# Kernel optimization log

Measured on AMD Instinct MI355X. Metric: run time of the kernel, lower is better.

Reference implementation:

```python
import jax, jax.numpy as jnp
import numpy as np

B, N, E, D, L = 32, 400, 200, 768, 3  # batch, max_entities, max_evidences, emb_dim, num_layers
_REL = ["ev_att", "ent_att", "ev_ent", "ent_ent", "ent_ev", "ev_ev"]


def setup_inputs() -> dict:
    key = jax.random.key(0)
    ks = jax.random.split(key, 20)
    s = 0.02
    inp = {
        "ent_emb": jax.random.normal(ks[0], (B, N, D), jnp.float32),
        "ev_emb": jax.random.normal(ks[1], (B, E, D), jnp.float32),
        "sr_vec": jax.random.normal(ks[2], (B, D), jnp.float32),
        "adj": (jax.random.uniform(ks[3], (B, E, N)) < 0.05).astype(jnp.float32),
    }
    for i, r in enumerate(_REL):
        inp[f"W_{r}"] = jax.random.normal(ks[4 + i], (L, D, D), jnp.float32) * s
        inp[f"b_{r}"] = jnp.zeros((L, D), jnp.float32)
    inp["W_ans"] = jax.random.normal(ks[10], (D, D), jnp.float32) * s
    inp["b_ans"] = jnp.zeros((), jnp.float32)
    inp["W_evb"] = jax.random.normal(ks[11], (D, D), jnp.float32) * s
    inp["b_evb"] = jnp.zeros((), jnp.float32)
    return inp


def _lin(x, W, b):
    return jnp.einsum('b...d,de->b...e', x, W) + b


def reference(ent_emb, ev_emb, sr_vec, adj,
              W_ev_att, b_ev_att, W_ent_att, b_ent_att,
              W_ev_ent, b_ev_ent, W_ent_ent, b_ent_ent,
              W_ent_ev, b_ent_ev, W_ev_ev, b_ev_ev,
              W_ans, b_ans, W_evb, b_evb):
    eps = 1e-9
    # degree-normalized adjacency: ev->ent aggregation and ent->ev aggregation
    adj_en = adj / (adj.sum(axis=1, keepdims=True) + eps)  # [B,E,N], norm over evidences
    adj_ne = adj / (adj.sum(axis=2, keepdims=True) + eps)  # [B,E,N], norm over entities
    ent, ev = ent_emb, ev_emb
    for i in range(L):
        # SR-conditioned attention over evidences / entities
        ev_att = jax.nn.softmax(jnp.einsum('bed,bd->be', _lin(ev, W_ev_att[i], b_ev_att[i]), sr_vec), axis=-1)   # [B,E]
        ent_att = jax.nn.softmax(jnp.einsum('bnd,bd->bn', _lin(ent, W_ent_att[i], b_ent_att[i]), sr_vec), axis=-1)  # [B,N]
        # relation-wise transform, attention-weight, scatter via adjacency
        ev_msg = _lin(ev, W_ev_ent[i], b_ev_ent[i]) * ev_att[..., None]    # [B,E,D]
        ent_msg = _lin(ent, W_ent_ev[i], b_ent_ev[i]) * ent_att[..., None]  # [B,N,D]
        ent_new = jax.nn.relu(_lin(ent, W_ent_ent[i], b_ent_ent[i]) + jnp.einsum('ben,bed->bnd', adj_en, ev_msg))
        ev_new = jax.nn.relu(_lin(ev, W_ev_ev[i], b_ev_ev[i]) + jnp.einsum('ben,bnd->bed', adj_ne, ent_msg))
        ent, ev = ent_new, ev_new
    # bilinear answering heads: x1 @ W @ x2 + b
    ans_logits = jnp.einsum('bnd,de,be->bn', ent, W_ans, sr_vec) + b_ans  # [B,N]
    ev_logits = jnp.einsum('bed,df,bf->be', ev, W_evb, sr_vec) + b_evb    # [B,E]
    return jnp.concatenate([ans_logits, ev_logits], axis=-1)  # [B, N+E]
```

## Files before the change

### kernel.cpp

```cpp
#include <hip/hip_runtime.h>
#include <cmath>

#define DD 768
#define BB 32
#define NN 400
#define EE 200
#define LL 3

#define KP1 224
#define KP2 416
#define AR1 512
#define AR2 256

typedef long long ll;
typedef _Float16 f16;
typedef f16 f16x8 __attribute__((ext_vector_type(8)));
typedef f16 f16x4 __attribute__((ext_vector_type(4)));
typedef float f32x4 __attribute__((ext_vector_type(4)));

template<int MROWS, int KPV>
__global__ __launch_bounds__(256)
void mfma_lin2(const f16* __restrict__ Ahi, const f16* __restrict__ Alo,
               const f16* __restrict__ Whs, const f16* __restrict__ Wls,
               const float* __restrict__ bs,
               const f16* __restrict__ Whm, const f16* __restrict__ Wlm,
               const float* __restrict__ bm,
               const float* __restrict__ rsc,
               float* __restrict__ C,
               f16* __restrict__ Th, f16* __restrict__ Tl)
{
    __shared__ __align__(16) union SM {
        struct { f16 As[2][128][40]; f16 Bs[2][128][40]; } k;
        f16 tb[128][160];
    } sm;
    auto& As = sm.k.As;
    auto& Bs = sm.k.Bs;

    const bool msg = (blockIdx.y >= DD / 128);
    const int n0 = (msg ? blockIdx.y - DD / 128 : blockIdx.y) * 128;
    const f16* __restrict__ Wh = msg ? Whm : Whs;
    const f16* __restrict__ Wl = msg ? Wlm : Wls;
    const float* __restrict__ bias = msg ? bm : bs;

    const int tid = threadIdx.x;
    const int lane = tid & 63, wid = tid >> 6;
    const int wr = wid >> 1, wc = wid & 1;
    const int l15 = lane & 15, lhi = lane >> 4;
    const int m0 = blockIdx.x * 128;
    const int srow = tid >> 2, sslot = tid & 3;

    f32x4 acc[4][4];
#pragma unroll
    for (int i = 0; i < 4; ++i)
#pragma unroll
        for (int j = 0; j < 4; ++j) acc[i][j] = (f32x4){0.f, 0.f, 0.f, 0.f};

    for (int k0 = 0; k0 < DD; k0 += 32) {
#pragma unroll
        for (int l = 0; l < 2; ++l) {
            const int row = srow + l * 64;
            const int kk = k0 + sslot * 8;
            const int4 va_h = *(const int4*)(Ahi + (ll)(m0 + row) * DD + kk);
            const int4 va_l = *(const int4*)(Alo + (ll)(m0 + row) * DD + kk);
            const int4 vb_h = *(const int4*)(Wh + (ll)(n0 + row) * DD + kk);
            const int4 vb_l = *(const int4*)(Wl + (ll)(n0 + row) * DD + kk);
            *(int4*)&As[0][row][sslot * 8] = va_h;
            *(int4*)&As[1][row][sslot * 8] = va_l;
            *(int4*)&Bs[0][row][sslot * 8] = vb_h;
            *(int4*)&Bs[1][row][sslot * 8] = vb_l;
        }
        __syncthreads();

        f16x8 ah[4], al[4];
#pragma unroll
        for (int m = 0; m < 4; ++m) {
            const int r = wr * 64 + m * 16 + l15;
            ah[m] = *(const f16x8*)&As[0][r][lhi * 8];
            al[m] = *(const f16x8*)&As[1][r][lhi * 8];
        }
#pragma unroll
        for (int n = 0; n < 4; ++n) {
            const int r = wc * 64 + n * 16 + l15;
            const f16x8 bh = *(const f16x8*)&Bs[0][r][lhi * 8];
            const f16x8 bl = *(const f16x8*)&Bs[1][r][lhi * 8];
#pragma unroll
            for (int m = 0; m < 4; ++m) {
                acc[m][n] = __builtin_amdgcn_mfma_f32_16x16x32_f16(ah[m], bh, acc[m][n], 0, 0, 0);
                acc[m][n] = __builtin_amdgcn_mfma_f32_16x16x32_f16(ah[m], bl, acc[m][n], 0, 0, 0);
                acc[m][n] = __builtin_amdgcn_mfma_f32_16x16x32_f16(al[m], bh, acc[m][n], 0, 0, 0);
            }
        }
        __syncthreads();
    }

#pragma unroll
    for (int m = 0; m < 4; ++m) {
        const int growb = m0 + wr * 64 + m * 16 + lhi * 4;
#pragma unroll
        for (int r = 0; r < 4; ++r) {
            const int grow = growb + r;
            const float rs = msg ? rsc[grow] : 1.f;
#pragma unroll
            for (int n = 0; n < 4; ++n) {
                const int gcol = n0 + wc * 64 + n * 16 + l15;
                float v = acc[m][n][r] + bias[gcol];
                if (msg) v *= rs;
                acc[m][n][r] = v;
                if (!msg) C[(ll)grow * DD + gcol] = v;
            }
        }
    }

    if (msg) {
        for (int ph = 0; ph < 2; ++ph) {
            __syncthreads();
#pragma unroll
            for (int m = 0; m < 4; ++m) {
#pragma unroll
                for (int n = 0; n < 4; ++n) {
                    const int col = wc * 64 + n * 16 + l15;
                    const int rowb = wr * 64 + m * 16 + lhi * 4;
                    f16x4 pv;
#pragma unroll
                    for (int r = 0; r < 4; ++r) {
                        const float v = acc[m][n][r];
                        const f16 h = (f16)v;
                        pv[r] = (ph == 0) ? h : (f16)(v - (float)h);
                    }
                    *(f16x4*)&sm.tb[col][rowb] = pv;
                }
            }
            __syncthreads();
            f16* T = ph ? Tl : Th;
            const int dl = tid >> 5;
            const int k4 = (tid & 31) * 4;
#pragma unroll
            for (int it = 0; it < 16; ++it) {
                const int d_local = dl + it * 8;
                const f16x4 v = *(const f16x4*)&sm.tb[d_local][k4];
                const int gk = m0 + k4;
                const int b = gk / MROWS;
                const int kk = gk - b * MROWS;
                *(f16x4*)(T + ((ll)b * DD + (n0 + d_local)) * KPV + kk) = v;
            }
        }
    }
}

template<bool EMIT_SPLIT>
__global__ __launch_bounds__(256)
void mfma_agg2(const f16* __restrict__ A1, const f16* __restrict__ B1h,
               const f16* __restrict__ B1l, const float* __restrict__ ds1,
               float* __restrict__ C1, f16* __restrict__ C1hi, f16* __restrict__ C1lo,
               const f16* __restrict__ A2, const f16* __restrict__ B2h,
               const f16* __restrict__ B2l, const float* __restrict__ ds2,
               float* __restrict__ C2, f16* __restrict__ C2hi, f16* __restrict__ C2lo)
{
    __shared__ __align__(16) f16 As[128][40];
    __shared__ __align__(16) f16 Bsh[128][40];
    __shared__ __align__(16) f16 Bsl[128][40];
    const int bz = blockIdx.z;
    const bool first = (blockIdx.x < AR1 / 128);

    const f16* A;
    const f16* Bh;
    const f16* Bl;
    const float* ds;
    float* C;
    f16* Chi;
    f16* Clo;
    int M, KP, m0;
    if (first) {
        A = A1 + (ll)bz * AR1 * KP1;
        Bh = B1h + (ll)bz * DD * KP1;
        Bl = B1l + (ll)bz * DD * KP1;
        ds = ds1 + (ll)bz * NN;
        C = C1 + (ll)bz * NN * DD;
        Chi = C1hi; Clo = C1lo;
        M = NN; KP = KP1;
        m0 = blockIdx.x * 128;
    } else {
        A = A2 + (ll)bz * AR2 * KP2;
        Bh = B2h + (ll)bz * DD * KP2;
        Bl = B2l + (ll)bz * DD * KP2;
        ds = ds2 + (ll)bz * EE;
        C = C2 + (ll)bz * EE * DD;
        Chi = C2hi; Clo = C2lo;
        M = EE; KP = KP2;
        m0 = (blockIdx.x - AR1 / 128) * 128;
    }

    const int tid = threadIdx.x;
    const int lane = tid & 63, wid = tid >> 6;
    const int wr = wid >> 1, wc = wid & 1;
    const int l15 = lane & 15, lhi = lane >> 4;
    const int n0 = blockIdx.y * 128;
    const int srow = tid >> 2, sslot = tid & 3;

    f32x4 acc[4][4];
#pragma unroll
    for (int i = 0; i < 4; ++i)
#pragma unroll
        for (int j = 0; j < 4; ++j) acc[i][j] = (f32x4){0.f, 0.f, 0.f, 0.f};

    for (int k0 = 0; k0 < KP; k0 += 32) {
#pragma unroll
        for (int l = 0; l < 2; ++l) {
            const int row = srow + l * 64;
            const int kk = k0 + sslot * 8;
            *(int4*)&As[row][sslot * 8]  = *(const int4*)(A  + (ll)(m0 + row) * KP + kk);
            *(int4*)&Bsh[row][sslot * 8] = *(const int4*)(Bh + (ll)(n0 + row) * KP + kk);
            *(int4*)&Bsl[row][sslot * 8] = *(const int4*)(Bl + (ll)(n0 + row) * KP + kk);
        }
        __syncthreads();

        f16x8 av[4];
#pragma unroll
        for (int m = 0; m < 4; ++m)
            av[m] = *(const f16x8*)&As[wr * 64 + m * 16 + l15][lhi * 8];
#pragma unroll
        for (int n = 0; n < 4; ++n) {
            const int r = wc * 64 + n * 16 + l15;
            const f16x8 bh = *(const f16x8*)&Bsh[r][lhi * 8];
            const f16x8 bl = *(const f16x8*)&Bsl[r][lhi * 8];
#pragma unroll
            for (int m = 0; m < 4; ++m) {
                acc[m][n] = __builtin_amdgcn_mfma_f32_16x16x32_f16(av[m], bh, acc[m][n], 0, 0, 0);
                acc[m][n] = __builtin_amdgcn_mfma_f32_16x16x32_f16(av[m], bl, acc[m][n], 0, 0, 0);
            }
        }
        __syncthreads();
    }

#pragma unroll
    for (int m = 0; m < 4; ++m) {
        const int growb = m0 + wr * 64 + m * 16 + lhi * 4;
#pragma unroll
        for (int r = 0; r < 4; ++r) {
            const int grow = growb + r;
            if (grow >= M) continue;
            const float rs = 1.f / (ds[grow] + 1e-9f);
#pragma unroll
            for (int n = 0; n < 4; ++n) {
                const int gcol = n0 + wc * 64 + n * 16 + l15;
                float v = acc[m][n][r] * rs + C[(ll)grow * DD + gcol];
                v = fmaxf(v, 0.f);
                C[(ll)grow * DD + gcol] = v;
                if (EMIT_SPLIT) {
                    const f16 h = (f16)v;
                    const ll oi = ((ll)bz * M + grow) * DD + gcol;
                    Chi[oi] = h;
                    Clo[oi] = (f16)(v - (float)h);
                }
            }
        }
    }
}

__global__ __launch_bounds__(256)
void split_f16(const float* __restrict__ x, f16* __restrict__ hi,
               f16* __restrict__ lo, ll n4)
{
    for (ll i = (ll)blockIdx.x * 256 + threadIdx.x; i < n4;
         i += (ll)gridDim.x * 256) {
        float4 v = ((const float4*)x)[i];
        f16 h0 = (f16)v.x, h1 = (f16)v.y, h2 = (f16)v.z, h3 = (f16)v.w;
        f16x4 hv = {h0, h1, h2, h3};
        f16x4 lv = {(f16)(v.x - (float)h0), (f16)(v.y - (float)h1),
                    (f16)(v.z - (float)h2), (f16)(v.w - (float)h3)};
        ((f16x4*)hi)[i] = hv;
        ((f16x4*)lo)[i] = lv;
    }
}

__global__ __launch_bounds__(256)
void adjprep(const float* __restrict__ adj, f16* __restrict__ adjF,
             f16* __restrict__ adjT)
{
    __shared__ float t[32][33];
    const int b = blockIdx.z;
    const int n0 = blockIdx.x * 32, e0 = blockIdx.y * 32;
    const int tx = threadIdx.x & 31, ty = threadIdx.x >> 5;
#pragma unroll
    for (int i = 0; i < 4; ++i) {
        const int e = e0 + ty + i * 8;
        const int n = n0 + tx;
        float v = 0.f;
        if (e < EE && n < NN) v = adj[((ll)b * EE + e) * NN + n];
        t[ty + i * 8][tx] = v;
        adjF[((ll)b * AR2 + e) * KP2 + n] = (f16)v;
    }
    __syncthreads();
#pragma unroll
    for (int i = 0; i < 4; ++i) {
        const int n = n0 + ty + i * 8;
        const int e = e0 + tx;
        adjT[((ll)b * AR1 + n) * KP1 + e] = (f16)t[tx][ty + i * 8];
    }
}

__global__ __launch_bounds__(256)
void wprep(const float* __restrict__ W0, const float* __restrict__ W1,
           const float* __restrict__ W2, const float* __restrict__ W3,
           f16* __restrict__ hi, f16* __restrict__ lo)
{
    __shared__ float t[32][33];
    const int mat = blockIdx.z;
    const float* Wb = mat < 3 ? W0 : mat < 6 ? W1 : mat < 9 ? W2 : W3;
    const float* W = Wb + (ll)(mat % 3) * DD * DD;
    f16* ho = hi + (ll)mat * DD * DD;
    f16* lp = lo + (ll)mat * DD * DD;
    const int tx = threadIdx.x & 31, ty = threadIdx.x >> 5;
    const int x0 = blockIdx.x * 32, y0 = blockIdx.y * 32;
#pragma unroll
    for (int i = 0; i < 4; ++i)
        t[ty + i * 8][tx] = W[(ll)(y0 + ty + i * 8) * DD + x0 + tx];
    __syncthreads();
#pragma unroll
    for (int i = 0; i < 4; ++i) {
        const float v = t[tx][ty + i * 8];
        const f16 h = (f16)v;
        const ll idx = (ll)(x0 + ty + i * 8) * DD + y0 + tx;
        ho[idx] = h;
        lp[idx] = (f16)(v - (float)h);
    }
}

__global__ __launch_bounds__(256)
void adj_sums(const float* __restrict__ adj, float* __restrict__ rowsum,
              float* __restrict__ colsum)
{
    const int b = blockIdx.x, tid = threadIdx.x;
    for (int e = tid; e < EE; e += 256) {
        const float* r = adj + ((ll)b * EE + e) * NN;
        float s = 0.f;
        for (int n = 0; n < NN; n += 4) {
            float4 v = *reinterpret_cast<const float4*>(r + n);
            s += v.x + v.y + v.z + v.w;
        }
        rowsum[b * EE + e] = s;
    }
    for (int n = tid; n < NN; n += 256) {
        float s = 0.f;
        for (int e = 0; e < EE; ++e) s += adj[((ll)b * EE + e) * NN + n];
        colsum[b * NN + n] = s;
    }
}

__global__ __launch_bounds__(256)
void attn2(const float* __restrict__ ev, const float* __restrict__ ent,
           const float* __restrict__ Wev, const float* __restrict__ bev,
           const float* __restrict__ Went, const float* __restrict__ bent,
           const float* __restrict__ sr,
           float* __restrict__ ev_att, float* __restrict__ ent_att)
{
    __shared__ float s_sr[DD];
    __shared__ float s_u[DD];
    __shared__ float s_log[NN];
    __shared__ float s_red[256];
    const int b = blockIdx.x, head = blockIdx.y, tid = threadIdx.x;
    const float* x = head ? ent : ev;
    const float* W = head ? Went : Wev;
    const float* bv = head ? bent : bev;
    float* att = head ? ent_att : ev_att;
    const int M = head ? NN : EE;

    for (int d = tid; d < DD; d += 256) s_sr[d] = sr[b * DD + d];
    __syncthreads();

    float cpart = 0.f;
    for (int d = tid; d < DD; d += 256) cpart += bv[d] * s_sr[d];
    for (int d = tid; d < DD; d += 256) {
        const float* wr = W + (ll)d * DD;
        float a = 0.f;
        for (int e = 0; e < DD; e += 4) {
            float4 w = *reinterpret_cast<const float4*>(wr + e);
            float4 s = *reinterpret_cast<const float4*>(s_sr + e);
            a += w.x * s.x + w.y * s.y + w.z * s.z + w.w * s.w;
        }
        s_u[d] = a;
    }
    s_red[tid] = cpart;
    __syncthreads();
    for (int off = 128; off > 0; off >>= 1) {
        if (tid < off) s_red[tid] += s_red[tid + off];
        __syncthreads();
    }
    const float c = s_red[0];
    __syncthreads();

    for (int m = tid; m < M; m += 256) {
        const float* xr = x + ((ll)b * M + m) * DD;
        float a = c;
        for (int e = 0; e < DD; e += 4) {
            float4 xv = *reinterpret_cast<const float4*>(xr + e);
            float4 uv = *reinterpret_cast<const float4*>(s_u + e);
            a += xv.x * uv.x + xv.y * uv.y + xv.z * uv.z + xv.w * uv.w;
        }
        s_log[m] = a;
    }
    __syncthreads();

    float mx = -1e30f;
    for (int m = tid; m < M; m += 256) mx = fmaxf(mx, s_log[m]);
    s_red[tid] = mx;
    __syncthreads();
    for (int off = 128; off > 0; off >>= 1) {
        if (tid < off) s_red[tid] = fmaxf(s_red[tid], s_red[tid + off]);
        __syncthreads();
    }
    const float smax = s_red[0];
    __syncthreads();

    float sum = 0.f;
    for (int m = tid; m < M; m += 256) {
        float e_ = expf(s_log[m] - smax);
        s_log[m] = e_;
        sum += e_;
    }
    s_red[tid] = sum;
    __syncthreads();
    for (int off = 128; off > 0; off >>= 1) {
        if (tid < off) s_red[tid] += s_red[tid + off];
        __syncthreads();
    }
    const float inv = 1.f / s_red[0];
    __syncthreads();
    for (int m = tid; m < M; m += 256) att[b * M + m] = s_log[m] * inv;
}

__global__ __launch_bounds__(256)
void heads_kernel(const float* __restrict__ ent, const float* __restrict__ ev,
                  const float* __restrict__ sr, const float* __restrict__ W_ans,
                  const float* __restrict__ b_ans, const float* __restrict__ W_evb,
                  const float* __restrict__ b_evb, float* __restrict__ out)
{
    __shared__ float s_sr[DD];
    __shared__ float s_v[DD];
    const int b = blockIdx.x, head = blockIdx.y, tid = threadIdx.x;
    const float* W = head ? W_evb : W_ans;
    const float* x = head ? ev : ent;
    const int M = head ? EE : NN;
    const float bias = head ? b_evb[0] : b_ans[0];
    float* o = out + (ll)b * (NN + EE) + (head ? NN : 0);

    for (int d = tid; d < DD; d += 256) s_sr[d] = sr[b * DD + d];
    __syncthreads();
    for (int d = tid; d < DD; d += 256) {
        const float* wr = W + (ll)d * DD;
        float a = 0.f;
        for (int e = 0; e < DD; e += 4) {
            float4 w = *reinterpret_cast<const float4*>(wr + e);
            float4 s = *reinterpret_cast<const float4*>(s_sr + e);
            a += w.x * s.x + w.y * s.y + w.z * s.z + w.w * s.w;
        }
        s_v[d] = a;
    }
    __syncthreads();
    for (int m = tid; m < M; m += 256) {
        const float* xr = x + ((ll)b * M + m) * DD;
        float a = bias;
        for (int e = 0; e < DD; e += 4) {
            float4 xv = *reinterpret_cast<const float4*>(xr + e);
            float4 vv = *reinterpret_cast<const float4*>(s_v + e);
            a += xv.x * vv.x + xv.y * vv.y + xv.z * vv.z + xv.w * vv.w;
        }
        o[m] = a;
    }
}

extern "C" void kernel_launch(void* const* d_in, const int* in_sizes, int n_in,
                              void* d_out, int out_size, void* d_ws, size_t ws_size,
                              hipStream_t stream)
{
    const float* ent_emb = (const float*)d_in[0];
    const float* ev_emb  = (const float*)d_in[1];
    const float* sr      = (const float*)d_in[2];
    const float* adj     = (const float*)d_in[3];
    const float* W_ev_att  = (const float*)d_in[4];
    const float* b_ev_att  = (const float*)d_in[5];
    const float* W_ent_att = (const float*)d_in[6];
    const float* b_ent_att = (const float*)d_in[7];
    const float* W_ev_ent  = (const float*)d_in[8];
    const float* b_ev_ent  = (const float*)d_in[9];
    const float* W_ent_ent = (const float*)d_in[10];
    const float* b_ent_ent = (const float*)d_in[11];
    const float* W_ent_ev  = (const float*)d_in[12];
    const float* b_ent_ev  = (const float*)d_in[13];
    const float* W_ev_ev   = (const float*)d_in[14];
    const float* b_ev_ev   = (const float*)d_in[15];
    const float* W_ans = (const float*)d_in[16];
    const float* b_ans = (const float*)d_in[17];
    const float* W_evb = (const float*)d_in[18];
    const float* b_evb = (const float*)d_in[19];

    float* ws = (float*)d_ws;
    ll o = 0;
    float* ent_ws = ws + o; o += (ll)BB * NN * DD;
    float* ev_ws  = ws + o; o += (ll)BB * EE * DD;
    float* ev_att  = ws + o; o += BB * EE;
    float* ent_att = ws + o; o += BB * NN;
    float* rowsum  = ws + o; o += BB * EE;
    float* colsum  = ws + o; o += BB * NN;
    o = (o + 3) & ~3LL;
    f16* fb = (f16*)(ws + o);
    ll o2 = 0;
    f16* enthi = fb + o2; o2 += (ll)BB * NN * DD;
    f16* entlo = fb + o2; o2 += (ll)BB * NN * DD;
    f16* evhi  = fb + o2; o2 += (ll)BB * EE * DD;
    f16* evlo  = fb + o2; o2 += (ll)BB * EE * DD;
    f16* WThi  = fb + o2; o2 += (ll)12 * DD * DD;
    f16* WTlo  = fb + o2; o2 += (ll)12 * DD * DD;
    f16* adjF  = fb + o2; o2 += (ll)BB * AR2 * KP2;
    f16* adjT  = fb + o2; o2 += (ll)BB * AR1 * KP1;
    f16* MevTh = fb + o2; o2 += (ll)BB * DD * KP1;
    f16* MevTl = fb + o2; o2 += (ll)BB * DD * KP1;
    f16* MentTh = fb + o2; o2 += (ll)BB * DD * KP2;
    f16* MentTl = fb + o2; o2 += (ll)BB * DD * KP2;

    const ll WS = (ll)DD * DD;
    const ll MS = (ll)DD * DD;

    adj_sums<<<BB, 256, 0, stream>>>(adj, rowsum, colsum);
    adjprep<<<dim3(KP2 / 32, KP1 / 32, BB), 256, 0, stream>>>(adj, adjF, adjT);
    wprep<<<dim3(DD / 32, DD / 32, 12), 256, 0, stream>>>(
        W_ev_ent, W_ent_ent, W_ent_ev, W_ev_ev, WThi, WTlo);
    split_f16<<<1024, 256, 0, stream>>>(ent_emb, enthi, entlo, (ll)BB * NN * DD / 4);
    split_f16<<<1024, 256, 0, stream>>>(ev_emb, evhi, evlo, (ll)BB * EE * DD / 4);

    const float* entc = ent_emb;
    const float* evc  = ev_emb;

    const dim3 gE2(BB * NN / 128, 2 * DD / 128);
    const dim3 gV2(BB * EE / 128, 2 * DD / 128);
    const dim3 gAm(AR1 / 128 + AR2 / 128, DD / 128, BB);

    for (int i = 0; i < LL; ++i) {
        attn2<<<dim3(BB, 2), 256, 0, stream>>>(
            evc, entc, W_ev_att + i * WS, b_ev_att + i * DD,
            W_ent_att + i * WS, b_ent_att + i * DD, sr, ev_att, ent_att);

        mfma_lin2<NN, KP2><<<gE2, 256, 0, stream>>>(
            enthi, entlo,
            WThi + (3 + i) * MS, WTlo + (3 + i) * MS, b_ent_ent + i * DD,
            WThi + (6 + i) * MS, WTlo + (6 + i) * MS, b_ent_ev + i * DD,
            ent_att, ent_ws, MentTh, MentTl);
        mfma_lin2<EE, KP1><<<gV2, 256, 0, stream>>>(
            evhi, evlo,
            WThi + (9 + i) * MS, WTlo + (9 + i) * MS, b_ev_ev + i * DD,
            WThi + (0 + i) * MS, WTlo + (0 + i) * MS, b_ev_ent + i * DD,
            ev_att, ev_ws, MevTh, MevTl);

        if (i < LL - 1) {
            mfma_agg2<true><<<gAm, 256, 0, stream>>>(
                adjT, MevTh, MevTl, colsum, ent_ws, enthi, entlo,
                adjF, MentTh, MentTl, rowsum, ev_ws, evhi, evlo);
        } else {
            mfma_agg2<false><<<gAm, 256, 0, stream>>>(
                adjT, MevTh, MevTl, colsum, ent_ws, nullptr, nullptr,
                adjF, MentTh, MentTl, rowsum, ev_ws, nullptr, nullptr);
        }

        entc = ent_ws;
        evc  = ev_ws;
    }

    heads_kernel<<<dim3(BB, 2), 256, 0, stream>>>(entc, evc, sr, W_ans, b_ans,
                                                  W_evb, b_evb, (float*)d_out);
}
```

Baseline: 1.763 ms.

## Merge ent/ev linear GEMMs into one launch and use direct global-to-LDS loads

The separate entity and evidence linear kernels become a single launch whose grid covers both, selecting operands per block. Both the linear and aggregation GEMMs now stage tiles with global_load_lds, writing straight into unpadded LDS instead of going through registers. This aims to cut register staging traffic and one launch per layer, and to let the two GEMMs share the GPU. The unpadded [128][32] LDS layout may cause bank conflicts on the fragment reads, and the wave-wide 16-byte LDS write pattern has to match the row layout exactly.

Measured after the change: 1.721 ms. 2.4% less time.

```diff
diff --git a/kernel.cpp b/kernel.cpp
--- a/kernel.cpp
+++ b/kernel.cpp
@@ -18,36 +18,55 @@
 typedef f16 f16x4 __attribute__((ext_vector_type(4)));
 typedef float f32x4 __attribute__((ext_vector_type(4)));
 
-template<int MROWS, int KPV>
-__global__ __launch_bounds__(256)
-void mfma_lin2(const f16* __restrict__ Ahi, const f16* __restrict__ Alo,
-               const f16* __restrict__ Whs, const f16* __restrict__ Wls,
-               const float* __restrict__ bs,
-               const f16* __restrict__ Whm, const f16* __restrict__ Wlm,
-               const float* __restrict__ bm,
-               const float* __restrict__ rsc,
-               float* __restrict__ C,
-               f16* __restrict__ Th, f16* __restrict__ Tl)
+__device__ __forceinline__ void gl16(const void* g, void* l) {
+    __builtin_amdgcn_global_load_lds(
+        (const __attribute__((address_space(1))) unsigned int*)g,
+        (__attribute__((address_space(3))) unsigned int*)l, 16, 0, 0);
+}
+
+__global__ __launch_bounds__(256)
+void mfma_lin4(const f16* __restrict__ entAh, const f16* __restrict__ entAl,
+               const f16* __restrict__ evAh,  const f16* __restrict__ evAl,
+               const f16* __restrict__ Wh_es, const f16* __restrict__ Wl_es,
+               const float* __restrict__ b_es,
+               const f16* __restrict__ Wh_em, const f16* __restrict__ Wl_em,
+               const float* __restrict__ b_em,
+               const f16* __restrict__ Wh_vs, const f16* __restrict__ Wl_vs,
+               const float* __restrict__ b_vs,
+               const f16* __restrict__ Wh_vm, const f16* __restrict__ Wl_vm,
+               const float* __restrict__ b_vm,
+               const float* __restrict__ ent_att, const float* __restrict__ ev_att,
+               float* __restrict__ Cent, float* __restrict__ Cev,
+               f16* __restrict__ TentH, f16* __restrict__ TentL,
+               f16* __restrict__ TevH,  f16* __restrict__ TevL)
 {
     __shared__ __align__(16) union SM {
-        struct { f16 As[2][128][40]; f16 Bs[2][128][40]; } k;
-        f16 tb[128][160];
+        f16 stg[4][128][32];
+        f16 tb[128][136];
     } sm;
-    auto& As = sm.k.As;
-    auto& Bs = sm.k.Bs;
-
+
+    const int bx = blockIdx.x;
+    const bool isEnt = bx < (BB * NN / 128);
+    const int xl = isEnt ? bx : bx - BB * NN / 128;
     const bool msg = (blockIdx.y >= DD / 128);
     const int n0 = (msg ? blockIdx.y - DD / 128 : blockIdx.y) * 128;
-    const f16* __restrict__ Wh = msg ? Whm : Whs;
-    const f16* __restrict__ Wl = msg ? Wlm : Wls;
-    const float* __restrict__ bias = msg ? bm : bs;
+    const int m0 = xl * 128;
+
+    const f16* __restrict__ Ah = isEnt ? entAh : evAh;
+    const f16* __restrict__ Al = isEnt ? entAl : evAl;
+    const f16* __restrict__ Wh = isEnt ? (msg ? Wh_em : Wh_es) : (msg ? Wh_vm : Wh_vs);
+    const f16* __restrict__ Wl = isEnt ? (msg ? Wl_em : Wl_es) : (msg ? Wl_vm : Wl_vs);
+    const float* __restrict__ bias = isEnt ? (msg ? b_em : b_es) : (msg ? b_vm : b_vs);
+    const float* __restrict__ rsc = isEnt ? ent_att : ev_att;
+    float* __restrict__ C = isEnt ? Cent : Cev;
 
     const int tid = threadIdx.x;
     const int lane = tid & 63, wid = tid >> 6;
     const int wr = wid >> 1, wc = wid & 1;
     const int l15 = lane & 15, lhi = lane >> 4;
-    const int m0 = blockIdx.x * 128;
-    const int srow = tid >> 2, sslot = tid & 3;
+    const int lr = lane >> 2;
+    const int lc = (lane & 3) * 8;
+    const int rb = wid * 32;
 
     f32x4 acc[4][4];
 #pragma unroll
@@ -56,33 +75,28 @@
         for (int j = 0; j < 4; ++j) acc[i][j] = (f32x4){0.f, 0.f, 0.f, 0.f};
 
     for (int k0 = 0; k0 < DD; k0 += 32) {
-#pragma unroll
-        for (int l = 0; l < 2; ++l) {
-            const int row = srow + l * 64;
-            const int kk = k0 + sslot * 8;
-            const int4 va_h = *(const int4*)(Ahi + (ll)(m0 + row) * DD + kk);
-            const int4 va_l = *(const int4*)(Alo + (ll)(m0 + row) * DD + kk);
-            const int4 vb_h = *(const int4*)(Wh + (ll)(n0 + row) * DD + kk);
-            const int4 vb_l = *(const int4*)(Wl + (ll)(n0 + row) * DD + kk);
-            *(int4*)&As[0][row][sslot * 8] = va_h;
-            *(int4*)&As[1][row][sslot * 8] = va_l;
-            *(int4*)&Bs[0][row][sslot * 8] = vb_h;
-            *(int4*)&Bs[1][row][sslot * 8] = vb_l;
-        }
+        gl16(Ah + (ll)(m0 + rb      + lr) * DD + k0 + lc, &sm.stg[0][rb     ][0]);
+        gl16(Ah + (ll)(m0 + rb + 16 + lr) * DD + k0 + lc, &sm.stg[0][rb + 16][0]);
+        gl16(Al + (ll)(m0 + rb      + lr) * DD + k0 + lc, &sm.stg[1][rb     ][0]);
+        gl16(Al + (ll)(m0 + rb + 16 + lr) * DD + k0 + lc, &sm.stg[1][rb + 16][0]);
+        gl16(Wh + (ll)(n0 + rb      + lr) * DD + k0 + lc, &sm.stg[2][rb     ][0]);
+        gl16(Wh + (ll)(n0 + rb + 16 + lr) * DD + k0 + lc, &sm.stg[2][rb + 16][0]);
+        gl16(Wl + (ll)(n0 + rb      + lr) * DD + k0 + lc, &sm.stg[3][rb     ][0]);
+        gl16(Wl + (ll)(n0 + rb + 16 + lr) * DD + k0 + lc, &sm.stg[3][rb + 16][0]);
         __syncthreads();
 
         f16x8 ah[4], al[4];
 #pragma unroll
         for (int m = 0; m < 4; ++m) {
             const int r = wr * 64 + m * 16 + l15;
-            ah[m] = *(const f16x8*)&As[0][r][lhi * 8];
-            al[m] = *(const f16x8*)&As[1][r][lhi * 8];
+            ah[m] = *(const f16x8*)&sm.stg[0][r][lhi * 8];
+            al[m] = *(const f16x8*)&sm.stg[1][r][lhi * 8];
         }
 #pragma unroll
         for (int n = 0; n < 4; ++n) {
             const int r = wc * 64 + n * 16 + l15;
-            const f16x8 bh = *(const f16x8*)&Bs[0][r][lhi * 8];
-            const f16x8 bl = *(const f16x8*)&Bs[1][r][lhi * 8];
+            const f16x8 bh = *(const f16x8*)&sm.stg[2][r][lhi * 8];
+            const f16x8 bl = *(const f16x8*)&sm.stg[3][r][lhi * 8];
 #pragma unroll
             for (int m = 0; m < 4; ++m) {
                 acc[m][n] = __builtin_amdgcn_mfma_f32_16x16x32_f16(ah[m], bh, acc[m][n], 0, 0, 0);
@@ -112,6 +126,9 @@
     }
 
     if (msg) {
+        f16* __restrict__ ThP = isEnt ? TentH : TevH;
+        f16* __restrict__ TlP = isEnt ? TentL : TevL;
+        const int KPV = isEnt ? KP2 : KP1;
         for (int ph = 0; ph < 2; ++ph) {
             __syncthreads();
 #pragma unroll
@@ -131,7 +148,7 @@
                 }
             }
             __syncthreads();
-            f16* T = ph ? Tl : Th;
+            f16* T = ph ? TlP : ThP;
             const int dl = tid >> 5;
             const int k4 = (tid & 31) * 4;
 #pragma unroll
@@ -139,8 +156,8 @@
                 const int d_local = dl + it * 8;
                 const f16x4 v = *(const f16x4*)&sm.tb[d_local][k4];
                 const int gk = m0 + k4;
-                const int b = gk / MROWS;
-                const int kk = gk - b * MROWS;
+                const int b = isEnt ? (gk / NN) : (gk / EE);
+                const int kk = gk - b * (isEnt ? NN : EE);
                 *(f16x4*)(T + ((ll)b * DD + (n0 + d_local)) * KPV + kk) = v;
             }
         }
@@ -156,9 +173,7 @@
                const f16* __restrict__ B2l, const float* __restrict__ ds2,
                float* __restrict__ C2, f16* __restrict__ C2hi, f16* __restrict__ C2lo)
 {
-    __shared__ __align__(16) f16 As[128][40];
-    __shared__ __align__(16) f16 Bsh[128][40];
-    __shared__ __align__(16) f16 Bsl[128][40];
+    __shared__ __align__(16) f16 stg[3][128][32];
     const int bz = blockIdx.z;
     const bool first = (blockIdx.x < AR1 / 128);
 
@@ -194,8 +209,9 @@
     const int lane = tid & 63, wid = tid >> 6;
     const int wr = wid >> 1, wc = wid & 1;
     const int l15 = lane & 15, lhi = lane >> 4;
+    const int lr = lane >> 2, lc = (lane & 3) * 8;
+    const int rb = wid * 32;
     const int n0 = blockIdx.y * 128;
-    const int srow = tid >> 2, sslot = tid & 3;
 
     f32x4 acc[4][4];
 #pragma unroll
@@ -204,25 +220,23 @@
         for (int j = 0; j < 4; ++j) acc[i][j] = (f32x4){0.f, 0.f, 0.f, 0.f};
 
     for (int k0 = 0; k0 < KP; k0 += 32) {
-#pragma unroll
-        for (int l = 0; l < 2; ++l) {
-            const int row = srow + l * 64;
-            const int kk = k0 + sslot * 8;
-            *(int4*)&As[row][sslot * 8]  = *(const int4*)(A  + (ll)(m0 + row) * KP + kk);
-            *(int4*)&Bsh[row][sslot * 8] = *(const int4*)(Bh + (ll)(n0 + row) * KP + kk);
-            *(int4*)&Bsl[row][sslot * 8] = *(const int4*)(Bl + (ll)(n0 + row) * KP + kk);
-        }
+        gl16(A  + (ll)(m0 + rb      + lr) * KP + k0 + lc, &stg[0][rb     ][0]);
+        gl16(A  + (ll)(m0 + rb + 16 + lr) * KP + k0 + lc, &stg[0][rb + 16][0]);
+        gl16(Bh + (ll)(n0 + rb      + lr) * KP + k0 + lc, &stg[1][rb     ][0]);
+        gl16(Bh + (ll)(n0 + rb + 16 + lr) * KP + k0 + lc, &stg[1][rb + 16][0]);
+        gl16(Bl + (ll)(n0 + rb      + lr) * KP + k0 + lc, &stg[2][rb     ][0]);
+        gl16(Bl + (ll)(n0 + rb + 16 + lr) * KP + k0 + lc, &stg[2][rb + 16][0]);
         __syncthreads();
 
         f16x8 av[4];
 #pragma unroll
         for (int m = 0; m < 4; ++m)
-            av[m] = *(const f16x8*)&As[wr * 64 + m * 16 + l15][lhi * 8];
+            av[m] = *(const f16x8*)&stg[0][wr * 64 + m * 16 + l15][lhi * 8];
 #pragma unroll
         for (int n = 0; n < 4; ++n) {
             const int r = wc * 64 + n * 16 + l15;
-            const f16x8 bh = *(const f16x8*)&Bsh[r][lhi * 8];
-            const f16x8 bl = *(const f16x8*)&Bsl[r][lhi * 8];
+            const f16x8 bh = *(const f16x8*)&stg[1][r][lhi * 8];
+            const f16x8 bl = *(const f16x8*)&stg[2][r][lhi * 8];
 #pragma unroll
             for (int m = 0; m < 4; ++m) {
                 acc[m][n] = __builtin_amdgcn_mfma_f32_16x16x32_f16(av[m], bh, acc[m][n], 0, 0, 0);
@@ -531,8 +545,7 @@
     const float* entc = ent_emb;
     const float* evc  = ev_emb;
 
-    const dim3 gE2(BB * NN / 128, 2 * DD / 128);
-    const dim3 gV2(BB * EE / 128, 2 * DD / 128);
+    const dim3 gL(BB * NN / 128 + BB * EE / 128, 2 * DD / 128);
     const dim3 gAm(AR1 / 128 + AR2 / 128, DD / 128, BB);
 
     for (int i = 0; i < LL; ++i) {
@@ -540,16 +553,14 @@
             evc, entc, W_ev_att + i * WS, b_ev_att + i * DD,
             W_ent_att + i * WS, b_ent_att + i * DD, sr, ev_att, ent_att);
 
-        mfma_lin2<NN, KP2><<<gE2, 256, 0, stream>>>(
-            enthi, entlo,
+        mfma_lin4<<<gL, 256, 0, stream>>>(
+            enthi, entlo, evhi, evlo,
             WThi + (3 + i) * MS, WTlo + (3 + i) * MS, b_ent_ent + i * DD,
             WThi + (6 + i) * MS, WTlo + (6 + i) * MS, b_ent_ev + i * DD,
-            ent_att, ent_ws, MentTh, MentTl);
-        mfma_lin2<EE, KP1><<<gV2, 256, 0, stream>>>(
-            evhi, evlo,
             WThi + (9 + i) * MS, WTlo + (9 + i) * MS, b_ev_ev + i * DD,
             WThi + (0 + i) * MS, WTlo + (0 + i) * MS, b_ev_ent + i * DD,
-            ev_att, ev_ws, MevTh, MevTl);
+            ent_att, ev_att, ent_ws, ev_ws,
+            MentTh, MentTl, MevTh, MevTl);
 
         if (i < LL - 1) {
             mfma_agg2<true><<<gAm, 256, 0, stream>>>(
```
